# Optimization experiments

Measured on AMD Instinct MI355X. Metric: run time of the kernel, lower is better.

The kernel has to match this reference:

```python
import jax, jax.numpy as jnp
import numpy as np

NEG_SLOPE = 0.2  # PyG GATConv default negative_slope


def gat_conv(x, src, dst, W, a_src, a_dst, b, concat):
    """One GATConv layer (PyG semantics, self-loops already in src/dst).
    x: [N, Fin]; src/dst: [E]; W: [Fin, H*C]; a_src/a_dst: [H, C]; b: [H*C] or [C].
    """
    N = x.shape[0]
    H, C = a_src.shape
    h = (x @ W).reshape(N, H, C)                     # [N, H, C]
    alpha_s = jnp.einsum('nhc,hc->nh', h, a_src)     # [N, H]
    alpha_d = jnp.einsum('nhc,hc->nh', h, a_dst)     # [N, H]
    e = alpha_s[src] + alpha_d[dst]                  # [E, H]
    e = jax.nn.leaky_relu(e, NEG_SLOPE)
    # scatter-softmax over edges sharing the same destination node
    m = jax.ops.segment_max(e, dst, num_segments=N)  # [N, H]
    e = jnp.exp(e - m[dst])
    denom = jax.ops.segment_sum(e, dst, num_segments=N)  # [N, H]
    alpha = e / (denom[dst] + 1e-16)                 # [E, H]
    msg = h[src] * alpha[:, :, None]                 # [E, H, C]
    out = jax.ops.segment_sum(msg, dst, num_segments=N)  # [N, H, C]
    out = out.reshape(N, H * C) if concat else out.mean(axis=1)
    return out + b


def setup_inputs() -> dict:
    key = jax.random.key(0)
    ks = jax.random.split(key, 8)
    N, E, Fin, Hid, Hds = 50000, 800000, 128, 64, 4
    x = jax.random.normal(ks[0], (N, Fin), dtype=jnp.float32)
    edge_index = jax.random.randint(ks[1], (2, E), 0, N, dtype=jnp.int64)
    s = 0.1
    return {
        'x': x,
        'edge_index': edge_index,
        'W1': jax.random.normal(ks[2], (Fin, Hds * Hid), dtype=jnp.float32) * s,
        'a_src1': jax.random.normal(ks[3], (Hds, Hid), dtype=jnp.float32) * s,
        'a_dst1': jax.random.normal(ks[4], (Hds, Hid), dtype=jnp.float32) * s,
        'b1': jnp.zeros((Hds * Hid,), dtype=jnp.float32),
        'W2': jax.random.normal(ks[5], (Hds * Hid, Hid), dtype=jnp.float32) * s,
        'a_src2': jax.random.normal(ks[6], (1, Hid), dtype=jnp.float32) * s,
        'a_dst2': jax.random.normal(ks[7], (1, Hid), dtype=jnp.float32) * s,
        'b2': jnp.zeros((Hid,), dtype=jnp.float32),
    }


def reference(x, edge_index, W1, a_src1, a_dst1, b1, W2, a_src2, a_dst2, b2):
    N = x.shape[0]
    # PyG GATConv add_self_loops=True: append (i, i) for every node
    loop = jnp.arange(N, dtype=edge_index.dtype)
    src = jnp.concatenate([edge_index[0], loop])
    dst = jnp.concatenate([edge_index[1], loop])
    h = gat_conv(x, src, dst, W1, a_src1, a_dst1, b1, concat=True)
    h = jax.nn.relu(h)  # dropout is identity in eval mode
    out = gat_conv(h, src, dst, W2, a_src2, a_dst2, b2, concat=False)
    return out
```

## Files before the change

### kernel.cpp

```cpp
#include <hip/hip_runtime.h>

#define LRELU(x) ((x) > 0.f ? (x) : 0.2f * (x))

typedef __attribute__((ext_vector_type(8))) short bf16x8;
typedef __attribute__((ext_vector_type(4))) float f32x4;

__device__ __forceinline__ unsigned short f2bf(float f) {
  unsigned int u = __float_as_uint(f);
  unsigned int r = (u + 0x7fffu + ((u >> 16) & 1u)) >> 16;
  return (unsigned short)r;
}
__device__ __forceinline__ float bf2f(unsigned short u) {
  return __uint_as_float(((unsigned int)u) << 16);
}
__device__ __forceinline__ float bflo(unsigned int u) { return __uint_as_float(u << 16); }
__device__ __forceinline__ float bfhi(unsigned int u) { return __uint_as_float(u & 0xffff0000u); }

__device__ __forceinline__ void lgkm0() { asm volatile("s_waitcnt lgkmcnt(0)" ::: "memory"); }

template <int NL>
__device__ __forceinline__ void wait_vmN() {
  if constexpr (NL == 2)      asm volatile("s_waitcnt vmcnt(2)" ::: "memory");
  else if constexpr (NL == 3) asm volatile("s_waitcnt vmcnt(3)" ::: "memory");
  else if constexpr (NL == 4) asm volatile("s_waitcnt vmcnt(4)" ::: "memory");
  else if constexpr (NL == 5) asm volatile("s_waitcnt vmcnt(5)" ::: "memory");
  else if constexpr (NL == 6) asm volatile("s_waitcnt vmcnt(6)" ::: "memory");
  else                        asm volatile("s_waitcnt vmcnt(0)" ::: "memory");
}
__device__ __forceinline__ void wait_vm0() { asm volatile("s_waitcnt vmcnt(0)" ::: "memory"); }

#define GLOAD_LDS16(g, l)                                                  \
  __builtin_amdgcn_global_load_lds(                                        \
      (const __attribute__((address_space(1))) void*)(g),                  \
      (__attribute__((address_space(3))) void*)(l), 16, 0, 0)

__device__ __forceinline__ int wave_detect64(const void* ei) {
  const int* w = (const int*)ei;
  int l = threadIdx.x & 63;
  int v = w[2 * l + 1] | w[2 * l + 129];
  return __ballot(v != 0) == 0ull;
}
__device__ __forceinline__ int edge_at(const void* ei, long long idx, int is64) {
  if (is64) return (int)((const long long*)ei)[idx];
  return ((const int*)ei)[idx];
}

__global__ __launch_bounds__(256) void prep_all(
    const float* __restrict__ x, unsigned short* __restrict__ xh, int n4,
    const float* __restrict__ W1, unsigned short* __restrict__ W1th,
    unsigned short* __restrict__ W1tl,
    const float* __restrict__ W2, unsigned short* __restrict__ W2th,
    unsigned short* __restrict__ W2tl,
    const void* __restrict__ ei, int* __restrict__ counts, int E, int N,
    int nbX, int nbW1, int nbW2) {
  int b = blockIdx.x;
  int tid = threadIdx.x;
  if (b < nbX) {
    int i = b * 256 + tid;
    if (i < n4) {
      float4 v = ((const float4*)x)[i];
      ushort4 h;
      h.x = f2bf(v.x); h.y = f2bf(v.y); h.z = f2bf(v.z); h.w = f2bf(v.w);
      ((ushort4*)xh)[i] = h;
    }
    return;
  }
  b -= nbX;
  if (b < nbW1) {
    int idx = b * 256 + tid;
    const int K = 128, Nc = 256;
    if (idx < K * Nc) {
      int n = idx / K, k = idx - n * K;
      float v = W1[(size_t)k * Nc + n];
      unsigned short h = f2bf(v);
      W1th[idx] = h;
      W1tl[idx] = f2bf(v - bf2f(h));
    }
    return;
  }
  b -= nbW1;
  if (b < nbW2) {
    int idx = b * 256 + tid;
    const int K = 256, Nc = 64;
    if (idx < K * Nc) {
      int n = idx / K, k = idx - n * K;
      float v = W2[(size_t)k * Nc + n];
      unsigned short h = f2bf(v);
      W2th[idx] = h;
      W2tl[idx] = f2bf(v - bf2f(h));
    }
    return;
  }
  b -= nbW2;
  int is64 = wave_detect64(ei);
  int i = b * 256 + tid;
  int tot = E + N;
  if (i >= tot) return;
  int d = (i < E) ? edge_at(ei, (long long)E + i, is64) : (i - E);
  atomicAdd(&counts[d], 1);
}

__global__ __launch_bounds__(512) void scan1_kernel(const int* __restrict__ counts,
                                                    int* __restrict__ partial,
                                                    int* __restrict__ blocksums, int N) {
  __shared__ int sm[1024];
  int t = threadIdx.x;
  int i = blockIdx.x * 512 + t;
  int v = (i < N) ? counts[i] : 0;
  int* cur = sm; int* nxt = sm + 512;
  cur[t] = v;
  __syncthreads();
  for (int off = 1; off < 512; off <<= 1) {
    int x = cur[t];
    if (t >= off) x += cur[t - off];
    nxt[t] = x;
    __syncthreads();
    int* tmp = cur; cur = nxt; nxt = tmp;
  }
  if (i < N) partial[i] = cur[t];
  if (t == 511) blocksums[blockIdx.x] = cur[511];
}

__global__ __launch_bounds__(256) void scan23_kernel(const int* __restrict__ partial,
                                                     const int* __restrict__ bs,
                                                     int* __restrict__ row_ptr,
                                                     int* __restrict__ cursor, int N, int SB) {
  __shared__ int bsp[128];
  int tid = threadIdx.x;
  if (tid < 64) {
    int l = tid;
    int a0 = (l < SB) ? bs[l] : 0;
    int a1 = (l + 64 < SB) ? bs[l + 64] : 0;
    int s0 = a0, s1 = a1;
#pragma unroll
    for (int o = 1; o < 64; o <<= 1) {
      int t0 = __shfl_up(s0, o);
      int t1 = __shfl_up(s1, o);
      if (l >= o) { s0 += t0; s1 += t1; }
    }
    int tot0 = __shfl(s0, 63);
    bsp[l] = s0 - a0;
    bsp[l + 64] = tot0 + s1 - a1;
  }
  __syncthreads();
  int i = blockIdx.x * 256 + tid;
  if (i == 0) { row_ptr[0] = 0; cursor[0] = 0; }
  if (i < N) {
    int v = partial[i] + bsp[i >> 9];
    row_ptr[i + 1] = v;
    if (i + 1 < N) cursor[i + 1] = v;
  }
}

__global__ void scatter_kernel(const void* __restrict__ ei,
                               int* __restrict__ cursor, int* __restrict__ srcs, int E, int N) {
  int is64 = wave_detect64(ei);
  int i = blockIdx.x * blockDim.x + threadIdx.x;
  int tot = E + N;
  if (i >= tot) return;
  int s, d;
  if (i < E) {
    s = edge_at(ei, i, is64);
    d = edge_at(ei, (long long)E + i, is64);
  } else {
    s = i - E; d = s;
  }
  int pos = atomicAdd(&cursor[d], 1);
  srcs[pos] = s;
}

template <int BROWS, int BCOLS, int WM, int WN, int H>
__global__ __launch_bounds__(256) void gemm_mfma(
    const unsigned short* __restrict__ A0, const unsigned short* __restrict__ B0,
    const unsigned short* __restrict__ B1, int M, int Ka,
    unsigned short* __restrict__ Cb, int ldc, const float* __restrict__ asrc,
    const float* __restrict__ adst, float* __restrict__ as, float* __restrict__ ad) {
  constexpr int WROWS = BROWS / WM;
  constexpr int WCOLS = BCOLS / WN;
  constexpr int MR = WROWS / 16;
  constexpr int NR = WCOLS / 16;
  constexpr int CH_A = BROWS / 64;
  constexpr int CH_B = BCOLS / 64;
  constexpr int NLOADS = CH_A + 2 * CH_B;
  __shared__ __align__(16) unsigned short Asm[2][4][BROWS][8];
  __shared__ __align__(16) unsigned short Bsm[2][2][4][BCOLS][8];
  int tid = threadIdx.x;
  int w = tid >> 6, l = tid & 63;
  int wm = w / WN, wn = w % WN;
  int l16 = l & 15, lg = l >> 4;
  int rowbase = blockIdx.y * BROWS;
  int colbase = blockIdx.x * BCOLS;
  int wrow = wm * WROWS, wcol = wn * WCOLS;
  const int KS = Ka / 32;

  auto stage = [&](int buf, int s) {
    int kk = s * 32;
#pragma unroll
    for (int q = 0; q < CH_A; ++q) {
      int i = q * 256 + tid;
      int p = i / BROWS, r = i % BROWS;
      int gr = rowbase + r;
      if (gr >= M) gr = M - 1;
      const unsigned short* src = A0 + (size_t)gr * Ka + kk + p * 8;
      unsigned short* dst = &Asm[buf][0][0][0] + ((size_t)q * 256 + (tid & ~63)) * 8;
      GLOAD_LDS16(src, dst);
    }
#pragma unroll
    for (int seg = 0; seg < 2; ++seg) {
      const unsigned short* Bp = seg ? B1 : B0;
#pragma unroll
      for (int q = 0; q < CH_B; ++q) {
        int i = q * 256 + tid;
        int p = i / BCOLS, r = i % BCOLS;
        const unsigned short* src = Bp + (size_t)(colbase + r) * Ka + kk + p * 8;
        unsigned short* dst = &Bsm[buf][seg][0][0][0] + ((size_t)q * 256 + (tid & ~63)) * 8;
        GLOAD_LDS16(src, dst);
      }
    }
  };

  f32x4 acc[MR][NR] = {};
  stage(0, 0);
  int buf = 0;
  for (int s = 0; s < KS; ++s) {
    if (s + 1 < KS) { stage(buf ^ 1, s + 1); wait_vmN<NLOADS>(); }
    else            { wait_vm0(); }
    __builtin_amdgcn_s_barrier();
    bf16x8 af[MR], bf0[NR], bf1[NR];
#pragma unroll
    for (int m = 0; m < MR; ++m) af[m] = *(const bf16x8*)&Asm[buf][lg][wrow + m * 16 + l16][0];
#pragma unroll
    for (int n = 0; n < NR; ++n) {
      bf0[n] = *(const bf16x8*)&Bsm[buf][0][lg][wcol + n * 16 + l16][0];
      bf1[n] = *(const bf16x8*)&Bsm[buf][1][lg][wcol + n * 16 + l16][0];
    }
#pragma unroll
    for (int m = 0; m < MR; ++m)
#pragma unroll
      for (int n = 0; n < NR; ++n)
        acc[m][n] = __builtin_amdgcn_mfma_f32_16x16x32_bf16(af[m], bf0[n], acc[m][n], 0, 0, 0);
#pragma unroll
    for (int m = 0; m < MR; ++m)
#pragma unroll
      for (int n = 0; n < NR; ++n)
        acc[m][n] = __builtin_amdgcn_mfma_f32_16x16x32_bf16(af[m], bf1[n], acc[m][n], 0, 0, 0);
    __builtin_amdgcn_s_barrier();
    buf ^= 1;
  }
#pragma unroll
  for (int m = 0; m < MR; ++m) {
    int r = rowbase + wrow + m * 16 + lg * 4;
#pragma unroll
    for (int n = 0; n < NR; ++n) {
      int c = colbase + wcol + n * 16 + l16;
#pragma unroll
      for (int j = 0; j < 4; ++j) {
        if (r + j < M) Cb[(size_t)(r + j) * ldc + c] = f2bf(acc[m][n][j]);
      }
    }
  }
  float asv[NR], adv_[NR];
#pragma unroll
  for (int n = 0; n < NR; ++n) {
    int c = colbase + wcol + n * 16 + l16;
    asv[n] = asrc[c];
    adv_[n] = adst[c];
  }
  int head = (H == 1) ? 0 : ((colbase + wcol) >> 6);
#pragma unroll
  for (int m = 0; m < MR; ++m) {
#pragma unroll
    for (int j = 0; j < 4; ++j) {
      float ps = 0.f, pd = 0.f;
#pragma unroll
      for (int n = 0; n < NR; ++n) {
        ps = fmaf(acc[m][n][j], asv[n], ps);
        pd = fmaf(acc[m][n][j], adv_[n], pd);
      }
#pragma unroll
      for (int o = 1; o < 16; o <<= 1) { ps += __shfl_xor(ps, o); pd += __shfl_xor(pd, o); }
      int r = rowbase + wrow + m * 16 + lg * 4 + j;
      if (l16 == 0 && r < M) {
        as[(size_t)r * H + head] = ps;
        ad[(size_t)r * H + head] = pd;
      }
    }
  }
}

__global__ __launch_bounds__(256) void agg4(const unsigned short* __restrict__ hb,
                                            const float* __restrict__ as,
                                            const float* __restrict__ ad,
                                            const int* __restrict__ row_ptr,
                                            const int* __restrict__ srcs,
                                            const float* __restrict__ bias,
                                            unsigned short* __restrict__ oh, int N) {
  __shared__ float els[4][128][4];
  __shared__ int   sls[4][128];
  int tid = threadIdx.x;
  int w = tid >> 6, l = tid & 63;
  int gw = (blockIdx.x << 2) + w;
  if (gw >= N) gw = N - 1;
  int g = l >> 4, p = l & 15;
  int beg = row_ptr[gw], end = row_ptr[gw + 1];
  float4 adv = *(const float4*)(ad + (size_t)gw * 4);
  float s0 = 0.f, s1 = 0.f, s2 = 0.f, s3 = 0.f;
  for (int j = beg + l; j < end; j += 64) {
    int sn = srcs[j];
    float4 a = *(const float4*)(as + (size_t)sn * 4);
    float x0 = __expf(LRELU(a.x + adv.x));
    float x1 = __expf(LRELU(a.y + adv.y));
    float x2 = __expf(LRELU(a.z + adv.z));
    float x3 = __expf(LRELU(a.w + adv.w));
    int slot = j - beg;
    if (slot < 128) {
      els[w][slot][0] = x0; els[w][slot][1] = x1;
      els[w][slot][2] = x2; els[w][slot][3] = x3;
      sls[w][slot] = sn;
    }
    s0 += x0; s1 += x1; s2 += x2; s3 += x3;
  }
#pragma unroll
  for (int o = 32; o; o >>= 1) {
    s0 += __shfl_xor(s0, o); s1 += __shfl_xor(s1, o);
    s2 += __shfl_xor(s2, o); s3 += __shfl_xor(s3, o);
  }
  float i0 = 1.f / (s0 + 1e-16f), i1 = 1.f / (s1 + 1e-16f);
  float i2 = 1.f / (s2 + 1e-16f), i3 = 1.f / (s3 + 1e-16f);
  int head = p >> 2;
  float Ih   = head == 0 ? i0 : head == 1 ? i1 : head == 2 ? i2 : i3;
  float advh = head == 0 ? adv.x : head == 1 ? adv.y : head == 2 ? adv.z : adv.w;
  lgkm0();
  float acc[16] = {};
  int jbase = beg + g;
  float xA = 0.f, xB = 0.f;
  uint4 vA0 = {}, vA1 = {}, vB0 = {}, vB1 = {};
  if (jbase < end) {
    int slot = jbase - beg;
    int sn;
    if (slot < 128) { sn = sls[w][slot]; xA = els[w][slot][head]; }
    else {
      sn = srcs[jbase];
      float4 a = *(const float4*)(as + (size_t)sn * 4);
      float ah = head == 0 ? a.x : head == 1 ? a.y : head == 2 ? a.z : a.w;
      xA = __expf(LRELU(ah + advh));
    }
    const unsigned short* hp = hb + (size_t)sn * 256 + p * 16;
    vA0 = *(const uint4*)(hp);
    vA1 = *(const uint4*)(hp + 8);
  }
  if (jbase + 4 < end) {
    int slot = jbase + 4 - beg;
    int sn;
    if (slot < 128) { sn = sls[w][slot]; xB = els[w][slot][head]; }
    else {
      sn = srcs[jbase + 4];
      float4 a = *(const float4*)(as + (size_t)sn * 4);
      float ah = head == 0 ? a.x : head == 1 ? a.y : head == 2 ? a.z : a.w;
      xB = __expf(LRELU(ah + advh));
    }
    const unsigned short* hp = hb + (size_t)sn * 256 + p * 16;
    vB0 = *(const uint4*)(hp);
    vB1 = *(const uint4*)(hp + 8);
  }
  for (int j = jbase; j < end; j += 4) {
    int jp = j + 8;
    float xC = 0.f; uint4 vC0 = {}, vC1 = {};
    if (jp < end) {
      int slot = jp - beg;
      int sn;
      if (slot < 128) { sn = sls[w][slot]; xC = els[w][slot][head]; }
      else {
        sn = srcs[jp];
        float4 a = *(const float4*)(as + (size_t)sn * 4);
        float ah = head == 0 ? a.x : head == 1 ? a.y : head == 2 ? a.z : a.w;
        xC = __expf(LRELU(ah + advh));
      }
      const unsigned short* hp = hb + (size_t)sn * 256 + p * 16;
      vC0 = *(const uint4*)(hp);
      vC1 = *(const uint4*)(hp + 8);
    }
    float al = xA * Ih;
    acc[0]  = fmaf(al, bflo(vA0.x), acc[0]);  acc[1]  = fmaf(al, bfhi(vA0.x), acc[1]);
    acc[2]  = fmaf(al, bflo(vA0.y), acc[2]);  acc[3]  = fmaf(al, bfhi(vA0.y), acc[3]);
    acc[4]  = fmaf(al, bflo(vA0.z), acc[4]);  acc[5]  = fmaf(al, bfhi(vA0.z), acc[5]);
    acc[6]  = fmaf(al, bflo(vA0.w), acc[6]);  acc[7]  = fmaf(al, bfhi(vA0.w), acc[7]);
    acc[8]  = fmaf(al, bflo(vA1.x), acc[8]);  acc[9]  = fmaf(al, bfhi(vA1.x), acc[9]);
    acc[10] = fmaf(al, bflo(vA1.y), acc[10]); acc[11] = fmaf(al, bfhi(vA1.y), acc[11]);
    acc[12] = fmaf(al, bflo(vA1.z), acc[12]); acc[13] = fmaf(al, bfhi(vA1.z), acc[13]);
    acc[14] = fmaf(al, bflo(vA1.w), acc[14]); acc[15] = fmaf(al, bfhi(vA1.w), acc[15]);
    xA = xB; vA0 = vB0; vA1 = vB1;
    xB = xC; vB0 = vC0; vB1 = vC1;
  }
#pragma unroll
  for (int i = 0; i < 16; ++i) acc[i] += __shfl_xor(acc[i], 16);
#pragma unroll
  for (int i = 0; i < 16; ++i) acc[i] += __shfl_xor(acc[i], 32);
  float o0 = g == 0 ? acc[0] : g == 1 ? acc[4]  : g == 2 ? acc[8]  : acc[12];
  float o1 = g == 0 ? acc[1] : g == 1 ? acc[5]  : g == 2 ? acc[9]  : acc[13];
  float o2 = g == 0 ? acc[2] : g == 1 ? acc[6]  : g == 2 ? acc[10] : acc[14];
  float o3 = g == 0 ? acc[3] : g == 1 ? acc[7]  : g == 2 ? acc[11] : acc[15];
  int c = p * 16 + g * 4;
  ushort4 ov;
  ov.x = f2bf(fmaxf(o0 + bias[c + 0], 0.f));
  ov.y = f2bf(fmaxf(o1 + bias[c + 1], 0.f));
  ov.z = f2bf(fmaxf(o2 + bias[c + 2], 0.f));
  ov.w = f2bf(fmaxf(o3 + bias[c + 3], 0.f));
  *(ushort4*)(oh + (size_t)gw * 256 + c) = ov;
}

__global__ __launch_bounds__(256) void agg1(const unsigned short* __restrict__ hb,
                                            const float* __restrict__ as,
                                            const float* __restrict__ ad,
                                            const int* __restrict__ row_ptr,
                                            const int* __restrict__ srcs,
                                            const float* __restrict__ bias,
                                            float* __restrict__ out, int N) {
  __shared__ float els[4][128];
  __shared__ int   sls[4][128];
  int tid = threadIdx.x;
  int w = tid >> 6, l = tid & 63;
  int gw = (blockIdx.x << 2) + w;
  if (gw >= N) gw = N - 1;
  int g = l >> 3, p = l & 7;
  int beg = row_ptr[gw], end = row_ptr[gw + 1];
  float adn = ad[gw];
  float s = 0.f;
  for (int j = beg + l; j < end; j += 64) {
    int sn = srcs[j];
    float x = __expf(LRELU(as[sn] + adn));
    int slot = j - beg;
    if (slot < 128) { els[w][slot] = x; sls[w][slot] = sn; }
    s += x;
  }
#pragma unroll
  for (int o = 32; o; o >>= 1) s += __shfl_xor(s, o);
  float inv = 1.f / (s + 1e-16f);
  lgkm0();
  float acc[8] = {};
  int jbase = beg + g;
  float xA = 0.f, xB = 0.f;
  uint4 vA = {}, vB = {};
  if (jbase < end) {
    int slot = jbase - beg;
    int sn;
    if (slot < 128) { sn = sls[w][slot]; xA = els[w][slot]; }
    else { sn = srcs[jbase]; xA = __expf(LRELU(as[sn] + adn)); }
    vA = *(const uint4*)(hb + (size_t)sn * 64 + p * 8);
  }
  if (jbase + 8 < end) {
    int slot = jbase + 8 - beg;
    int sn;
    if (slot < 128) { sn = sls[w][slot]; xB = els[w][slot]; }
    else { sn = srcs[jbase + 8]; xB = __expf(LRELU(as[sn] + adn)); }
    vB = *(const uint4*)(hb + (size_t)sn * 64 + p * 8);
  }
  for (int j = jbase; j < end; j += 8) {
    int jp = j + 16;
    float xC = 0.f; uint4 vC = {};
    if (jp < end) {
      int slot = jp - beg;
      int sn;
      if (slot < 128) { sn = sls[w][slot]; xC = els[w][slot]; }
      else { sn = srcs[jp]; xC = __expf(LRELU(as[sn] + adn)); }
      vC = *(const uint4*)(hb + (size_t)sn * 64 + p * 8);
    }
    float al = xA * inv;
    acc[0] = fmaf(al, bflo(vA.x), acc[0]); acc[1] = fmaf(al, bfhi(vA.x), acc[1]);
    acc[2] = fmaf(al, bflo(vA.y), acc[2]); acc[3] = fmaf(al, bfhi(vA.y), acc[3]);
    acc[4] = fmaf(al, bflo(vA.z), acc[4]); acc[5] = fmaf(al, bfhi(vA.z), acc[5]);
    acc[6] = fmaf(al, bflo(vA.w), acc[6]); acc[7] = fmaf(al, bfhi(vA.w), acc[7]);
    xA = xB; vA = vB;
    xB = xC; vB = vC;
  }
#pragma unroll
  for (int i = 0; i < 8; ++i) acc[i] += __shfl_xor(acc[i], 8);
#pragma unroll
  for (int i = 0; i < 8; ++i) acc[i] += __shfl_xor(acc[i], 16);
#pragma unroll
  for (int i = 0; i < 8; ++i) acc[i] += __shfl_xor(acc[i], 32);
  float ov = g == 0 ? acc[0] : g == 1 ? acc[1] : g == 2 ? acc[2] : g == 3 ? acc[3]
           : g == 4 ? acc[4] : g == 5 ? acc[5] : g == 6 ? acc[6] : acc[7];
  int c = p * 8 + g;
  out[(size_t)gw * 64 + c] = ov + bias[c];
}

extern "C" void kernel_launch(void* const* d_in, const int* in_sizes, int n_in,
                              void* d_out, int out_size, void* d_ws, size_t ws_size,
                              hipStream_t stream) {
  const float* x      = (const float*)d_in[0];
  const void*  ei     = d_in[1];
  const float* W1     = (const float*)d_in[2];
  const float* a_src1 = (const float*)d_in[3];
  const float* a_dst1 = (const float*)d_in[4];
  const float* b1     = (const float*)d_in[5];
  const float* W2     = (const float*)d_in[6];
  const float* a_src2 = (const float*)d_in[7];
  const float* a_dst2 = (const float*)d_in[8];
  const float* b2     = (const float*)d_in[9];

  const int Fin = 128;
  const int N   = in_sizes[0] / Fin;
  const int E   = in_sizes[1] / 2;
  const int HC1 = in_sizes[2] / Fin;
  const int Etot = E + N;

  char* wp = (char*)d_ws;
  auto alloc = [&](size_t bytes) {
    void* p = (void*)wp;
    wp += (bytes + 255) & ~(size_t)255;
    return p;
  };
  int* counts    = (int*)alloc((size_t)N * 4);
  int* row_ptr   = (int*)alloc((size_t)(N + 1) * 4);
  int* cursor    = (int*)alloc((size_t)N * 4);
  int* partial   = (int*)alloc((size_t)N * 4);
  int* blocksums = (int*)alloc(4096);
  int* srcs      = (int*)alloc((size_t)Etot * 4);
  unsigned short* xh   = (unsigned short*)alloc((size_t)N * Fin * 2);
  unsigned short* xpad = (unsigned short*)alloc((size_t)N * Fin * 2);
  unsigned short* W1th = (unsigned short*)alloc((size_t)HC1 * Fin * 2);
  unsigned short* W1tl = (unsigned short*)alloc((size_t)HC1 * Fin * 2);
  unsigned short* W2th = (unsigned short*)alloc((size_t)64 * HC1 * 2);
  unsigned short* W2tl = (unsigned short*)alloc((size_t)64 * HC1 * 2);
  unsigned short* h1b  = (unsigned short*)alloc((size_t)N * 256 * 2);
  float* as1 = (float*)alloc((size_t)N * 4 * 4);
  float* ad1 = (float*)alloc((size_t)N * 4 * 4);
  float* as2 = (float*)alloc((size_t)N * 4);
  float* ad2 = (float*)alloc((size_t)N * 4);
  (void)xpad;
  unsigned short* o1h = xh;
  unsigned short* h2b = h1b;

  const int SB = (N + 511) / 512;
  const int n4 = N * Fin / 4;
  const int nbX  = (n4 + 255) / 256;
  const int nbW1 = (Fin * HC1 + 255) / 256;
  const int nbW2 = (HC1 * 64 + 255) / 256;
  const int nbH  = (Etot + 255) / 256;

  hipMemsetAsync(counts, 0, (size_t)N * 4, stream);
  prep_all<<<nbX + nbW1 + nbW2 + nbH, 256, 0, stream>>>(
      x, xh, n4, W1, W1th, W1tl, W2, W2th, W2tl, ei, counts, E, N, nbX, nbW1, nbW2);

  scan1_kernel<<<SB, 512, 0, stream>>>(counts, partial, blocksums, N);
  scan23_kernel<<<(N + 255) / 256, 256, 0, stream>>>(partial, blocksums, row_ptr, cursor, N, SB);
  scatter_kernel<<<(Etot + 255) / 256, 256, 0, stream>>>(ei, cursor, srcs, E, N);

  gemm_mfma<128, 128, 2, 2, 4><<<dim3(2, (N + 127) / 128), 256, 0, stream>>>(
      xh, W1th, W1tl, N, Fin, h1b, 256, a_src1, a_dst1, as1, ad1);
  agg4<<<(N + 3) / 4, 256, 0, stream>>>(h1b, as1, ad1, row_ptr, srcs, b1, o1h, N);

  gemm_mfma<64, 64, 4, 1, 1><<<dim3(1, (N + 63) / 64), 256, 0, stream>>>(
      o1h, W2th, W2tl, N, HC1, h2b, 64, a_src2, a_dst2, as2, ad2);
  agg1<<<(N + 3) / 4, 256, 0, stream>>>(h2b, as2, ad2, row_ptr, srcs, b2, (float*)d_out, N);
}
```

Before: 241.8 us.

## Split layer-1 aggregation into edge-alpha pass and column-sliced gather kernel

The fused agg4 kernel is replaced by two kernels. alpha_edge computes normalized per-edge attention weights and writes them to a new global buffer. agg4s then gathers neighbour features in 8 column slices of 32 channels, using a grid dimension over slices so each wave handles one slice of one node. The aim is more parallelism and smaller per-thread register state in the gather. In exchange it adds an extra kernel launch and an E*4 float write and read, re-reads srcs and row_ptr 8 times, and uses narrow 4-byte gathers instead of 32-byte vector loads.

```diff
diff --git a/kernel.cpp b/kernel.cpp
--- a/kernel.cpp
+++ b/kernel.cpp
@@ -288,20 +288,16 @@
   }
 }
 
-__global__ __launch_bounds__(256) void agg4(const unsigned short* __restrict__ hb,
-                                            const float* __restrict__ as,
-                                            const float* __restrict__ ad,
-                                            const int* __restrict__ row_ptr,
-                                            const int* __restrict__ srcs,
-                                            const float* __restrict__ bias,
-                                            unsigned short* __restrict__ oh, int N) {
+__global__ __launch_bounds__(256) void alpha_edge(const float* __restrict__ as,
+                                                  const float* __restrict__ ad,
+                                                  const int* __restrict__ row_ptr,
+                                                  const int* __restrict__ srcs,
+                                                  float* __restrict__ ae, int N) {
   __shared__ float els[4][128][4];
-  __shared__ int   sls[4][128];
   int tid = threadIdx.x;
   int w = tid >> 6, l = tid & 63;
   int gw = (blockIdx.x << 2) + w;
   if (gw >= N) gw = N - 1;
-  int g = l >> 4, p = l & 15;
   int beg = row_ptr[gw], end = row_ptr[gw + 1];
   float4 adv = *(const float4*)(ad + (size_t)gw * 4);
   float s0 = 0.f, s1 = 0.f, s2 = 0.f, s3 = 0.f;
@@ -316,7 +312,6 @@
     if (slot < 128) {
       els[w][slot][0] = x0; els[w][slot][1] = x1;
       els[w][slot][2] = x2; els[w][slot][3] = x3;
-      sls[w][slot] = sn;
     }
     s0 += x0; s1 += x1; s2 += x2; s3 += x3;
   }
@@ -327,86 +322,70 @@
   }
   float i0 = 1.f / (s0 + 1e-16f), i1 = 1.f / (s1 + 1e-16f);
   float i2 = 1.f / (s2 + 1e-16f), i3 = 1.f / (s3 + 1e-16f);
-  int head = p >> 2;
-  float Ih   = head == 0 ? i0 : head == 1 ? i1 : head == 2 ? i2 : i3;
-  float advh = head == 0 ? adv.x : head == 1 ? adv.y : head == 2 ? adv.z : adv.w;
   lgkm0();
-  float acc[16] = {};
-  int jbase = beg + g;
-  float xA = 0.f, xB = 0.f;
-  uint4 vA0 = {}, vA1 = {}, vB0 = {}, vB1 = {};
-  if (jbase < end) {
-    int slot = jbase - beg;
-    int sn;
-    if (slot < 128) { sn = sls[w][slot]; xA = els[w][slot][head]; }
-    else {
-      sn = srcs[jbase];
+  for (int j = beg + l; j < end; j += 64) {
+    int slot = j - beg;
+    float x0, x1, x2, x3;
+    if (slot < 128) {
+      x0 = els[w][slot][0]; x1 = els[w][slot][1];
+      x2 = els[w][slot][2]; x3 = els[w][slot][3];
+    } else {
+      int sn = srcs[j];
       float4 a = *(const float4*)(as + (size_t)sn * 4);
-      float ah = head == 0 ? a.x : head == 1 ? a.y : head == 2 ? a.z : a.w;
-      xA = __expf(LRELU(ah + advh));
-    }
-    const unsigned short* hp = hb + (size_t)sn * 256 + p * 16;
-    vA0 = *(const uint4*)(hp);
-    vA1 = *(const uint4*)(hp + 8);
-  }
-  if (jbase + 4 < end) {
-    int slot = jbase + 4 - beg;
-    int sn;
-    if (slot < 128) { sn = sls[w][slot]; xB = els[w][slot][head]; }
-    else {
-      sn = srcs[jbase + 4];
-      float4 a = *(const float4*)(as + (size_t)sn * 4);
-      float ah = head == 0 ? a.x : head == 1 ? a.y : head == 2 ? a.z : a.w;
-      xB = __expf(LRELU(ah + advh));
-    }
-    const unsigned short* hp = hb + (size_t)sn * 256 + p * 16;
-    vB0 = *(const uint4*)(hp);
-    vB1 = *(const uint4*)(hp + 8);
-  }
-  for (int j = jbase; j < end; j += 4) {
-    int jp = j + 8;
-    float xC = 0.f; uint4 vC0 = {}, vC1 = {};
-    if (jp < end) {
-      int slot = jp - beg;
-      int sn;
-      if (slot < 128) { sn = sls[w][slot]; xC = els[w][slot][head]; }
-      else {
-        sn = srcs[jp];
-        float4 a = *(const float4*)(as + (size_t)sn * 4);
-        float ah = head == 0 ? a.x : head == 1 ? a.y : head == 2 ? a.z : a.w;
-        xC = __expf(LRELU(ah + advh));
-      }
-      const unsigned short* hp = hb + (size_t)sn * 256 + p * 16;
-      vC0 = *(const uint4*)(hp);
-      vC1 = *(const uint4*)(hp + 8);
-    }
-    float al = xA * Ih;
-    acc[0]  = fmaf(al, bflo(vA0.x), acc[0]);  acc[1]  = fmaf(al, bfhi(vA0.x), acc[1]);
-    acc[2]  = fmaf(al, bflo(vA0.y), acc[2]);  acc[3]  = fmaf(al, bfhi(vA0.y), acc[3]);
-    acc[4]  = fmaf(al, bflo(vA0.z), acc[4]);  acc[5]  = fmaf(al, bfhi(vA0.z), acc[5]);
-    acc[6]  = fmaf(al, bflo(vA0.w), acc[6]);  acc[7]  = fmaf(al, bfhi(vA0.w), acc[7]);
-    acc[8]  = fmaf(al, bflo(vA1.x), acc[8]);  acc[9]  = fmaf(al, bfhi(vA1.x), acc[9]);
-    acc[10] = fmaf(al, bflo(vA1.y), acc[10]); acc[11] = fmaf(al, bfhi(vA1.y), acc[11]);
-    acc[12] = fmaf(al, bflo(vA1.z), acc[12]); acc[13] = fmaf(al, bfhi(vA1.z), acc[13]);
-    acc[14] = fmaf(al, bflo(vA1.w), acc[14]); acc[15] = fmaf(al, bfhi(vA1.w), acc[15]);
-    xA = xB; vA0 = vB0; vA1 = vB1;
-    xB = xC; vB0 = vC0; vB1 = vC1;
-  }
-#pragma unroll
-  for (int i = 0; i < 16; ++i) acc[i] += __shfl_xor(acc[i], 16);
-#pragma unroll
-  for (int i = 0; i < 16; ++i) acc[i] += __shfl_xor(acc[i], 32);
-  float o0 = g == 0 ? acc[0] : g == 1 ? acc[4]  : g == 2 ? acc[8]  : acc[12];
-  float o1 = g == 0 ? acc[1] : g == 1 ? acc[5]  : g == 2 ? acc[9]  : acc[13];
-  float o2 = g == 0 ? acc[2] : g == 1 ? acc[6]  : g == 2 ? acc[10] : acc[14];
-  float o3 = g == 0 ? acc[3] : g == 1 ? acc[7]  : g == 2 ? acc[11] : acc[15];
-  int c = p * 16 + g * 4;
-  ushort4 ov;
-  ov.x = f2bf(fmaxf(o0 + bias[c + 0], 0.f));
-  ov.y = f2bf(fmaxf(o1 + bias[c + 1], 0.f));
-  ov.z = f2bf(fmaxf(o2 + bias[c + 2], 0.f));
-  ov.w = f2bf(fmaxf(o3 + bias[c + 3], 0.f));
-  *(ushort4*)(oh + (size_t)gw * 256 + c) = ov;
+      x0 = __expf(LRELU(a.x + adv.x));
+      x1 = __expf(LRELU(a.y + adv.y));
+      x2 = __expf(LRELU(a.z + adv.z));
+      x3 = __expf(LRELU(a.w + adv.w));
+    }
+    float4 o = make_float4(x0 * i0, x1 * i1, x2 * i2, x3 * i3);
+    *(float4*)(ae + (size_t)j * 4) = o;
+  }
+}
+
+__global__ __launch_bounds__(256) void agg4s(const unsigned short* __restrict__ hb,
+                                             const float* __restrict__ ae,
+                                             const int* __restrict__ row_ptr,
+                                             const int* __restrict__ srcs,
+                                             const float* __restrict__ bias,
+                                             unsigned short* __restrict__ oh, int N) {
+  int tid = threadIdx.x;
+  int w = tid >> 6, l = tid & 63;
+  int gw = (blockIdx.y << 2) + w;
+  if (gw >= N) gw = N - 1;
+  int s = blockIdx.x;
+  int head = s >> 1;
+  int g = l >> 4, p = l & 15;
+  int beg = row_ptr[gw], end = row_ptr[gw + 1];
+  const unsigned short* hbase = hb + (size_t)s * 32 + p * 2;
+  float a0 = 0.f, a1 = 0.f;
+  int j = beg + g;
+  float xA = 0.f; unsigned int vA = 0;
+  if (j < end) {
+    int sn = srcs[j];
+    xA = ae[(size_t)j * 4 + head];
+    vA = *(const unsigned int*)(hbase + (size_t)sn * 256);
+  }
+  while (j < end) {
+    int jn = j + 4;
+    float xB = 0.f; unsigned int vB = 0;
+    if (jn < end) {
+      int sn = srcs[jn];
+      xB = ae[(size_t)jn * 4 + head];
+      vB = *(const unsigned int*)(hbase + (size_t)sn * 256);
+    }
+    a0 = fmaf(xA, bflo(vA), a0);
+    a1 = fmaf(xA, bfhi(vA), a1);
+    j = jn; xA = xB; vA = vB;
+  }
+  a0 += __shfl_xor(a0, 16); a1 += __shfl_xor(a1, 16);
+  a0 += __shfl_xor(a0, 32); a1 += __shfl_xor(a1, 32);
+  if (g == 0) {
+    int c = s * 32 + p * 2;
+    float o0 = fmaxf(a0 + bias[c], 0.f);
+    float o1 = fmaxf(a1 + bias[c + 1], 0.f);
+    unsigned int pk = ((unsigned int)f2bf(o1) << 16) | (unsigned int)f2bf(o0);
+    *(unsigned int*)(oh + (size_t)gw * 256 + c) = pk;
+  }
 }
 
 __global__ __launch_bounds__(256) void agg1(const unsigned short* __restrict__ hb,
@@ -528,6 +507,7 @@
   float* ad1 = (float*)alloc((size_t)N * 4 * 4);
   float* as2 = (float*)alloc((size_t)N * 4);
   float* ad2 = (float*)alloc((size_t)N * 4);
+  float* ae  = (float*)alloc((size_t)Etot * 4 * 4);
   (void)xpad;
   unsigned short* o1h = xh;
   unsigned short* h2b = h1b;
@@ -549,7 +529,8 @@
 
   gemm_mfma<128, 128, 2, 2, 4><<<dim3(2, (N + 127) / 128), 256, 0, stream>>>(
       xh, W1th, W1tl, N, Fin, h1b, 256, a_src1, a_dst1, as1, ad1);
-  agg4<<<(N + 3) / 4, 256, 0, stream>>>(h1b, as1, ad1, row_ptr, srcs, b1, o1h, N);
+  alpha_edge<<<(N + 3) / 4, 256, 0, stream>>>(as1, ad1, row_ptr, srcs, ae, N);
+  agg4s<<<dim3(8, (N + 3) / 4), 256, 0, stream>>>(h1b, ae, row_ptr, srcs, b1, o1h, N);
 
   gemm_mfma<64, 64, 4, 1, 1><<<dim3(1, (N + 63) / 64), 256, 0, stream>>>(
       o1h, W2th, W2tl, N, HC1, h2b, 64, a_src2, a_dst2, as2, ad2);
```

After: 397.7 us. 1.64x slower.
